# Kernel optimization log

Hardware: AMD Instinct MI355X
Metric: run time of the kernel (lower is better)

Reference implementation:

```python
import jax, jax.numpy as jnp
import numpy as np

OUT_FEATURES = 4096
IN_FEATURES = 4096
GROUP_SIZE = 128
N_GROUPS = OUT_FEATURES * IN_FEATURES // GROUP_SIZE  # 131072


def setup_inputs() -> dict:
    key = jax.random.key(0)
    k_x, k_t, k_s = jax.random.split(key, 3)
    x = jax.random.normal(k_x, (4, 2048, IN_FEATURES), dtype=jnp.float32)
    # ternary codes in {-1, 0, 1}, stored as int (int8 in the original module)
    ternary = jax.random.randint(k_t, (OUT_FEATURES, IN_FEATURES), 0, 3, dtype=jnp.int32) - 1
    # per-group positive scales (beta = mean |w| per group in the original init)
    scales = jax.random.uniform(k_s, (N_GROUPS,), dtype=jnp.float32, minval=0.01, maxval=0.1)
    return {"x": x, "ternary": ternary, "scales": scales}


def reference(x, ternary, scales):
    # Dequantize: expand per-group scale across group_size, multiply ternary sign.
    w = (ternary.astype(jnp.float32).reshape(-1, GROUP_SIZE) * scales[:, None])
    w = w.reshape(OUT_FEATURES, IN_FEATURES)
    # F.linear(x, W) = x @ W.T
    return jnp.einsum('bsi,oi->bso', x, w)
```

## Files before the change

### kernel.cpp

```cpp
#include <hip/hip_runtime.h>
#include <hip/hip_bf16.h>


#define Msz 8192
#define Nsz 4096
#define Ksz 4096

typedef __attribute__((ext_vector_type(8))) short short8;
typedef __attribute__((ext_vector_type(4))) float f32x4;
typedef __attribute__((ext_vector_type(4))) int int4v;
typedef __attribute__((ext_vector_type(4))) float float4v;
typedef __attribute__((ext_vector_type(8))) unsigned short ushort8;

static __device__ __forceinline__ unsigned short f2bf(float f) {
    unsigned u = __builtin_bit_cast(unsigned, f);
    u += 0x7fffu + ((u >> 16) & 1u);
    return (unsigned short)(u >> 16);
}

__global__ void prep(const float* __restrict__ x, const int* __restrict__ t,
                     const float* __restrict__ s,
                     unsigned short* __restrict__ ox, unsigned short* __restrict__ ow) {
    if (blockIdx.x < 2048) {
        int i = blockIdx.x * 256 + threadIdx.x;
        for (; i < Msz * Ksz / 8; i += 2048 * 256) {
            const float4v* p = (const float4v*)x + (size_t)i * 2;
            float4v a = p[0], b = p[1];
            ushort8 r;
            r[0] = f2bf(a[0]); r[1] = f2bf(a[1]); r[2] = f2bf(a[2]); r[3] = f2bf(a[3]);
            r[4] = f2bf(b[0]); r[5] = f2bf(b[1]); r[6] = f2bf(b[2]); r[7] = f2bf(b[3]);
            *((ushort8*)ox + i) = r;
        }
    } else {
        int i = (blockIdx.x - 2048) * 256 + threadIdx.x;
        for (; i < Nsz * Ksz / 8; i += 1024 * 256) {
            float sc = s[i >> 4];
            const int4v* p = (const int4v*)t + (size_t)i * 2;
            int4v a = p[0], b = p[1];
            ushort8 r;
            r[0] = f2bf((float)a[0] * sc); r[1] = f2bf((float)a[1] * sc);
            r[2] = f2bf((float)a[2] * sc); r[3] = f2bf((float)a[3] * sc);
            r[4] = f2bf((float)b[0] * sc); r[5] = f2bf((float)b[1] * sc);
            r[6] = f2bf((float)b[2] * sc); r[7] = f2bf((float)b[3] * sc);
            *((ushort8*)ow + i) = r;
        }
    }
}


#define READ_Bv(b) {                                                             \
    _Pragma("unroll") for (int n = 0; n < 4; ++n)                                \
    _Pragma("unroll") for (int ks = 0; ks < 2; ++ks)                             \
      bfr[n][ks] = *(const short8*)(L + (b)*65536 + 32768 + ((((wc)*4+n)*2+ks)<<10) + laneA); }

#define READ_Aq(S, b, q) {                                                       \
    _Pragma("unroll") for (int m = 0; m < 2; ++m)                                \
    _Pragma("unroll") for (int ks = 0; ks < 2; ++ks)                             \
      S[m][ks] = *(const short8*)(L + (b)*65536 + ((((q)*4+(wr)*2+m)*2+ks)<<10) + laneA); }

#define MFMAS_Q(q, AF) {                                                         \
    _Pragma("unroll") for (int m = 0; m < 2; ++m)                                \
    _Pragma("unroll") for (int n = 0; n < 4; ++n) {                              \
      acc[(q)*2+m][n] = __builtin_amdgcn_mfma_f32_16x16x32_bf16(AF[m][0], bfr[n][0], acc[(q)*2+m][n], 0, 0, 0); \
      acc[(q)*2+m][n] = __builtin_amdgcn_mfma_f32_16x16x32_bf16(AF[m][1], bfr[n][1], acc[(q)*2+m][n], 0, 0, 0); } }

#define STAGE_H(PM, MOFF, BOFF, T, H) {                                          \
    _Pragma("unroll") for (int j = 0; j < 2; ++j)                                \
      __builtin_amdgcn_global_load_lds(                                          \
        (const __attribute__((address_space(1))) void*)(PM + (size_t)((H)*128 + j*64)*Ksz + (T)*64), \
        (__attribute__((address_space(3))) void*)(L + (BOFF) + (MOFF) + (H)*16384 + j*8192 + dOff), \
        16, 0, 0); }

#define BAR_ONLY                                                                 \
    __builtin_amdgcn_sched_barrier(0);                                           \
    __builtin_amdgcn_s_barrier();                                                \
    __builtin_amdgcn_sched_barrier(0);

#define BAR_V6                                                                   \
    __builtin_amdgcn_sched_barrier(0);                                           \
    asm volatile("s_waitcnt vmcnt(6)" ::: "memory");                             \
    __builtin_amdgcn_s_barrier();                                                \
    __builtin_amdgcn_sched_barrier(0);

#define SECTION(b, TA1, TBA)                                                     \
    STAGE_H(pAb, 0, (1-(b))*65536, TA1, 1);                                      \
    READ_Bv(b);                                                                  \
    READ_Aq(afA, b, 0);                                                          \
    READ_Aq(afB, b, 1);                                                          \
    __builtin_amdgcn_s_setprio(1);                                               \
    MFMAS_Q(0, afA);                                                             \
    MFMAS_Q(1, afB);                                                             \
    __builtin_amdgcn_s_setprio(0);                                               \
    BAR_ONLY                                                                     \
    STAGE_H(pBb, 32768, (b)*65536, TBA, 0);                                      \
    STAGE_H(pBb, 32768, (b)*65536, TBA, 1);                                      \
    STAGE_H(pAb, 0,     (b)*65536, TBA, 0);                                      \
    READ_Aq(afA, b, 2);                                                          \
    READ_Aq(afB, b, 3);                                                          \
    __builtin_amdgcn_s_setprio(1);                                               \
    MFMAS_Q(2, afA);                                                             \
    MFMAS_Q(3, afB);                                                             \
    __builtin_amdgcn_s_setprio(0);                                               \
    BAR_V6

__global__ __launch_bounds__(512, 2) void gemm_8p(const unsigned short* __restrict__ A,
                                                  const unsigned short* __restrict__ B,
                                                  float* __restrict__ C) {
    __shared__ __align__(16) unsigned char L[131072];

    const int tid  = threadIdx.x;
    const int lane = tid & 63;
    const int wid  = tid >> 6;
    const int wr   = wid >> 2;
    const int wc   = wid & 3;
    const int rowBase = blockIdx.y * 256;
    const int colBase = blockIdx.x * 256;

    const int laneA = (((lane & 15) * 64) + ((lane >> 4) * 16)) ^ (((lane >> 3) & 1) << 5);
    const int kloc = (lane & 1) * 8 + (((lane >> 1) ^ (lane >> 5)) & 1) * 16;
    const int r_st = lane >> 2;
    const int dOff = wid * 1024;

    const unsigned short* pAb = A + (size_t)(rowBase + (wid >> 1) * 16 + r_st) * Ksz + (wid & 1) * 32 + kloc;
    const unsigned short* pBb = B + (size_t)(colBase + (wid >> 1) * 16 + r_st) * Ksz + (wid & 1) * 32 + kloc;

    f32x4 acc[8][4] = {};
    short8 afA[2][2], afB[2][2], bfr[4][2];

    STAGE_H(pBb, 32768, 0,     0, 0);
    STAGE_H(pBb, 32768, 0,     0, 1);
    STAGE_H(pAb, 0,     0,     0, 0);
    STAGE_H(pAb, 0,     0,     0, 1);
    STAGE_H(pBb, 32768, 65536, 1, 0);
    STAGE_H(pBb, 32768, 65536, 1, 1);
    STAGE_H(pAb, 0,     65536, 1, 0);
    STAGE_H(pAb, 0,     65536, 1, 1);
    __builtin_amdgcn_sched_barrier(0);
    asm volatile("s_waitcnt vmcnt(8)" ::: "memory");
    __builtin_amdgcn_s_barrier();
    __builtin_amdgcn_sched_barrier(0);

    for (int i = 0; i < 32; ++i) {
        const int t1 = 2 * i + 1;
        const int t2 = (i < 31) ? 2 * i + 2 : 62;
        const int t3 = (i < 31) ? 2 * i + 3 : 62;

        SECTION(0, t1, t2)
        SECTION(1, t2, t3)
    }

    asm volatile("s_waitcnt vmcnt(0) lgkmcnt(0)" ::: "memory");

    const int crl = (lane >> 4) * 4;
    const int ccol0 = colBase + wc * 64 + (lane & 15);
#pragma unroll
    for (int q = 0; q < 4; ++q)
#pragma unroll
        for (int m = 0; m < 2; ++m)
#pragma unroll
            for (int n = 0; n < 4; ++n) {
                const int row0 = rowBase + (q * 4 + wr * 2 + m) * 16 + crl;
                float* cp = C + (size_t)row0 * Nsz + ccol0 + n * 16;
#pragma unroll
                for (int j = 0; j < 4; ++j)
                    cp[(size_t)j * Nsz] = acc[q * 2 + m][n][j];
            }
}

__global__ void gemm_naive(const float* __restrict__ x, const int* __restrict__ t,
                           const float* __restrict__ s, float* __restrict__ C) {
    size_t o = (size_t)blockIdx.x * blockDim.x + threadIdx.x;
    if (o >= (size_t)Msz * Nsz) return;
    int m = (int)(o / Nsz), n = (int)(o % Nsz);
    float acc = 0.f;
    for (int g = 0; g < Ksz / 128; ++g) {
        float sc = s[n * (Ksz / 128) + g];
        float p = 0.f;
        const float* xp = x + (size_t)m * Ksz + g * 128;
        const int* tp = t + (size_t)n * Ksz + g * 128;
        for (int k = 0; k < 128; ++k) p += xp[k] * (float)tp[k];
        acc += sc * p;
    }
    C[o] = acc;
}

extern "C" void kernel_launch(void* const* d_in, const int* in_sizes, int n_in,
                              void* d_out, int out_size, void* d_ws, size_t ws_size,
                              hipStream_t stream) {
    const float* x      = (const float*)d_in[0];
    const int*   tern   = (const int*)d_in[1];
    const float* scales = (const float*)d_in[2];
    float* out = (float*)d_out;

    const size_t aBytes = (size_t)Msz * Ksz * 2;
    const size_t bBytes = (size_t)Nsz * Ksz * 2;

    if (ws_size >= aBytes + bBytes) {
        unsigned short* Abf = (unsigned short*)d_ws;
        unsigned short* Bbf = (unsigned short*)((char*)d_ws + aBytes);
        prep<<<3072, 256, 0, stream>>>(x, tern, scales, Abf, Bbf);
        dim3 grid(Nsz / 256, Msz / 256);
        gemm_8p<<<grid, 512, 0, stream>>>(Abf, Bbf, out);
    } else {
        gemm_naive<<<(int)(((size_t)Msz * Nsz + 255) / 256), 256, 0, stream>>>(x, tern, scales, out);
    }
}
```

Measured before the change: 266.6 us.

## Load B fragments directly from global into registers, halve LDS footprint

The GEMM stops staging B tiles through LDS and has each wave load its B fragments straight from global memory into double-buffered registers (BE/BO), while A stays in LDS through global_load_lds. LDS drops from 128KB to 64KB per block, which could allow more blocks per CU, and the B LDS writes and reads disappear. The grid mapping is also swapped so blockIdx.x walks M, which changes L2 reuse of the B tiles. In exchange, B global reads are no longer coalesced across the block and each wave column re-reads the same B rows, and the vmcnt wait accounting becomes more fragile.

```diff
diff --git a/kernel.cpp b/kernel.cpp
--- a/kernel.cpp
+++ b/kernel.cpp
@@ -48,73 +48,71 @@
 }
 
 
-#define READ_Bv(b) {                                                             \
-    _Pragma("unroll") for (int n = 0; n < 4; ++n)                                \
-    _Pragma("unroll") for (int ks = 0; ks < 2; ++ks)                             \
-      bfr[n][ks] = *(const short8*)(L + (b)*65536 + 32768 + ((((wc)*4+n)*2+ks)<<10) + laneA); }
-
 #define READ_Aq(S, b, q) {                                                       \
     _Pragma("unroll") for (int m = 0; m < 2; ++m)                                \
     _Pragma("unroll") for (int ks = 0; ks < 2; ++ks)                             \
-      S[m][ks] = *(const short8*)(L + (b)*65536 + ((((q)*4+(wr)*2+m)*2+ks)<<10) + laneA); }
-
-#define MFMAS_Q(q, AF) {                                                         \
+      S[m][ks] = *(const short8*)(L + (b)*32768 + ((((q)*4+(wr)*2+m)*2+ks)<<10) + laneA); }
+
+#define MFMAS_Q(q, AF, BF) {                                                     \
     _Pragma("unroll") for (int m = 0; m < 2; ++m)                                \
     _Pragma("unroll") for (int n = 0; n < 4; ++n) {                              \
-      acc[(q)*2+m][n] = __builtin_amdgcn_mfma_f32_16x16x32_bf16(AF[m][0], bfr[n][0], acc[(q)*2+m][n], 0, 0, 0); \
-      acc[(q)*2+m][n] = __builtin_amdgcn_mfma_f32_16x16x32_bf16(AF[m][1], bfr[n][1], acc[(q)*2+m][n], 0, 0, 0); } }
-
-#define STAGE_H(PM, MOFF, BOFF, T, H) {                                          \
+      acc[(q)*2+m][n] = __builtin_amdgcn_mfma_f32_16x16x32_bf16(AF[m][0], BF[n][0], acc[(q)*2+m][n], 0, 0, 0); \
+      acc[(q)*2+m][n] = __builtin_amdgcn_mfma_f32_16x16x32_bf16(AF[m][1], BF[n][1], acc[(q)*2+m][n], 0, 0, 0); } }
+
+#define LOAD_B(S, T) {                                                           \
+    _Pragma("unroll") for (int n = 0; n < 4; ++n)                                \
+    _Pragma("unroll") for (int ks = 0; ks < 2; ++ks)                             \
+      S[n][ks] = *(const short8*)(pB + (size_t)(n) * 16 * Ksz + (ks) * 32 + (size_t)(T) * 64); }
+
+#define STAGE_A(BOFF, T, H) {                                                    \
     _Pragma("unroll") for (int j = 0; j < 2; ++j)                                \
       __builtin_amdgcn_global_load_lds(                                          \
-        (const __attribute__((address_space(1))) void*)(PM + (size_t)((H)*128 + j*64)*Ksz + (T)*64), \
-        (__attribute__((address_space(3))) void*)(L + (BOFF) + (MOFF) + (H)*16384 + j*8192 + dOff), \
+        (const __attribute__((address_space(1))) void*)(pAb + (size_t)((H)*128 + j*64)*Ksz + (size_t)(T)*64), \
+        (__attribute__((address_space(3))) void*)(L + (BOFF) + (H)*16384 + j*8192 + dOff), \
         16, 0, 0); }
 
-#define BAR_ONLY                                                                 \
-    __builtin_amdgcn_sched_barrier(0);                                           \
-    __builtin_amdgcn_s_barrier();                                                \
-    __builtin_amdgcn_sched_barrier(0);
-
-#define BAR_V6                                                                   \
-    __builtin_amdgcn_sched_barrier(0);                                           \
-    asm volatile("s_waitcnt vmcnt(6)" ::: "memory");                             \
-    __builtin_amdgcn_s_barrier();                                                \
-    __builtin_amdgcn_sched_barrier(0);
-
-#define SECTION(b, TA1, TBA)                                                     \
-    STAGE_H(pAb, 0, (1-(b))*65536, TA1, 1);                                      \
-    READ_Bv(b);                                                                  \
+#define SBAR __builtin_amdgcn_sched_barrier(0);
+
+#define BAR_ONLY  SBAR __builtin_amdgcn_s_barrier(); SBAR
+
+#define BAR_V10                                                                  \
+    SBAR asm volatile("s_waitcnt vmcnt(10)" ::: "memory");                       \
+    __builtin_amdgcn_s_barrier(); SBAR
+
+#define SECTION(b, BF, BFN, TB, TAH1, TAH0)                                      \
+    STAGE_A((1-(b))*32768, TAH1, 1);                                             \
+    SBAR                                                                         \
+    LOAD_B(BFN, TB);                                                             \
+    SBAR                                                                         \
     READ_Aq(afA, b, 0);                                                          \
     READ_Aq(afB, b, 1);                                                          \
     __builtin_amdgcn_s_setprio(1);                                               \
-    MFMAS_Q(0, afA);                                                             \
-    MFMAS_Q(1, afB);                                                             \
+    MFMAS_Q(0, afA, BF);                                                         \
+    MFMAS_Q(1, afB, BF);                                                         \
     __builtin_amdgcn_s_setprio(0);                                               \
     BAR_ONLY                                                                     \
-    STAGE_H(pBb, 32768, (b)*65536, TBA, 0);                                      \
-    STAGE_H(pBb, 32768, (b)*65536, TBA, 1);                                      \
-    STAGE_H(pAb, 0,     (b)*65536, TBA, 0);                                      \
+    STAGE_A((b)*32768, TAH0, 0);                                                 \
+    SBAR                                                                         \
     READ_Aq(afA, b, 2);                                                          \
     READ_Aq(afB, b, 3);                                                          \
     __builtin_amdgcn_s_setprio(1);                                               \
-    MFMAS_Q(2, afA);                                                             \
-    MFMAS_Q(3, afB);                                                             \
+    MFMAS_Q(2, afA, BF);                                                         \
+    MFMAS_Q(3, afB, BF);                                                         \
     __builtin_amdgcn_s_setprio(0);                                               \
-    BAR_V6
+    BAR_V10
 
 __global__ __launch_bounds__(512, 2) void gemm_8p(const unsigned short* __restrict__ A,
                                                   const unsigned short* __restrict__ B,
                                                   float* __restrict__ C) {
-    __shared__ __align__(16) unsigned char L[131072];
+    __shared__ __align__(16) unsigned char L[65536];
 
     const int tid  = threadIdx.x;
     const int lane = tid & 63;
     const int wid  = tid >> 6;
     const int wr   = wid >> 2;
     const int wc   = wid & 3;
-    const int rowBase = blockIdx.y * 256;
-    const int colBase = blockIdx.x * 256;
+    const int rowBase = blockIdx.x * 256;
+    const int colBase = blockIdx.y * 256;
 
     const int laneA = (((lane & 15) * 64) + ((lane >> 4) * 16)) ^ (((lane >> 3) & 1) << 5);
     const int kloc = (lane & 1) * 8 + (((lane >> 1) ^ (lane >> 5)) & 1) * 16;
@@ -122,31 +120,31 @@
     const int dOff = wid * 1024;
 
     const unsigned short* pAb = A + (size_t)(rowBase + (wid >> 1) * 16 + r_st) * Ksz + (wid & 1) * 32 + kloc;
-    const unsigned short* pBb = B + (size_t)(colBase + (wid >> 1) * 16 + r_st) * Ksz + (wid & 1) * 32 + kloc;
+    const unsigned short* pB  = B + (size_t)(colBase + wc * 64 + (lane & 15)) * Ksz + (lane >> 4) * 8;
 
     f32x4 acc[8][4] = {};
-    short8 afA[2][2], afB[2][2], bfr[4][2];
-
-    STAGE_H(pBb, 32768, 0,     0, 0);
-    STAGE_H(pBb, 32768, 0,     0, 1);
-    STAGE_H(pAb, 0,     0,     0, 0);
-    STAGE_H(pAb, 0,     0,     0, 1);
-    STAGE_H(pBb, 32768, 65536, 1, 0);
-    STAGE_H(pBb, 32768, 65536, 1, 1);
-    STAGE_H(pAb, 0,     65536, 1, 0);
-    STAGE_H(pAb, 0,     65536, 1, 1);
-    __builtin_amdgcn_sched_barrier(0);
-    asm volatile("s_waitcnt vmcnt(8)" ::: "memory");
+    short8 afA[2][2], afB[2][2], BE[4][2], BO[4][2];
+
+    STAGE_A(0, 0, 0);
+    STAGE_A(0, 0, 1);
+    SBAR
+    LOAD_B(BE, 0);
+    SBAR
+    STAGE_A(32768, 1, 0);
+    SBAR
+    asm volatile("s_waitcnt vmcnt(2)" ::: "memory");
     __builtin_amdgcn_s_barrier();
-    __builtin_amdgcn_sched_barrier(0);
+    SBAR
 
     for (int i = 0; i < 32; ++i) {
-        const int t1 = 2 * i + 1;
-        const int t2 = (i < 31) ? 2 * i + 2 : 62;
-        const int t3 = (i < 31) ? 2 * i + 3 : 62;
-
-        SECTION(0, t1, t2)
-        SECTION(1, t2, t3)
+        const int e  = 2 * i;
+        const int tb_o  = (i < 31) ? e + 2 : 63;
+        const int ta1_o = (i < 31) ? e + 2 : 63;
+        const int ta0_e = (i < 31) ? e + 2 : 63;
+        const int ta0_o = (i < 31) ? e + 3 : 63;
+
+        SECTION(0, BE, BO, e + 1, e + 1, ta0_e)
+        SECTION(1, BO, BE, tb_o, ta1_o, ta0_o)
     }
 
     asm volatile("s_waitcnt vmcnt(0) lgkmcnt(0)" ::: "memory");
@@ -199,7 +197,7 @@
         unsigned short* Abf = (unsigned short*)d_ws;
         unsigned short* Bbf = (unsigned short*)((char*)d_ws + aBytes);
         prep<<<3072, 256, 0, stream>>>(x, tern, scales, Abf, Bbf);
-        dim3 grid(Nsz / 256, Msz / 256);
+        dim3 grid(Msz / 256, Nsz / 256);
         gemm_8p<<<grid, 512, 0, stream>>>(Abf, Bbf, out);
     } else {
         gemm_naive<<<(int)(((size_t)Msz * Nsz + 255) / 256), 256, 0, stream>>>(x, tern, scales, out);
```

New measurement: 405.3 us. 1.52x slower.
